# Performance work log

Measured on AMD Instinct MI355X. Metric: run time of the kernel, lower is better.

The kernel has to match this reference:

```python
import math
import jax, jax.numpy as jnp
import numpy as np

B, LA, LB, H = 16, 1024, 1024, 512
NEG = -10000000.0


def setup_inputs() -> dict:
    key = jax.random.key(0)
    k1, k2, k3, k4 = jax.random.split(key, 4)
    a = jax.random.normal(k1, (B, LA, H), dtype=jnp.float32)
    b = jax.random.normal(k2, (B, LB, H), dtype=jnp.float32)
    mask_a = jax.random.randint(k3, (B, LA, 1), 0, 2, dtype=jnp.int32)
    mask_b = jax.random.randint(k4, (B, LB, 1), 0, 2, dtype=jnp.int32)
    temperature = jnp.asarray(1.0 / math.sqrt(H), dtype=jnp.float32)
    return {"a": a, "b": b, "mask_a": mask_a, "mask_b": mask_b, "temperature": temperature}


def reference(a, b, mask_a, mask_b, temperature):
    # attn[b,i,j] = <a_i, b_j> * temperature  -> [B, LA, LB]
    attn = jnp.einsum("bid,bjd->bij", a, b) * temperature
    # pairwise validity mask: outer product of per-token masks
    mask = jnp.einsum("bik,bjk->bij", mask_a.astype(jnp.float32), mask_b.astype(jnp.float32)) > 0
    attn = jnp.where(mask, attn, NEG)
    attn_a = jax.nn.softmax(attn, axis=1)  # softmax over a-tokens
    attn_b = jax.nn.softmax(attn, axis=2)  # softmax over b-tokens
    feature_b = jnp.einsum("bij,bid->bjd", attn_a, a)  # [B, LB, H]
    feature_a = jnp.einsum("bij,bjd->bid", attn_b, b)  # [B, LA, H]
    return (feature_a, feature_b)
```

## Files before the change

### kernel.cpp

```cpp
#include <hip/hip_runtime.h>
#include <hip/hip_bf16.h>

#define NB_ 16
#define LA_ 1024
#define LB_ 1024
#define H_  512

typedef __attribute__((ext_vector_type(8))) short short8;
typedef __attribute__((ext_vector_type(4))) float f32x4;

using bf16 = __hip_bfloat16;

__device__ __forceinline__ float bf2f(unsigned short u) {
    union { unsigned int i; float f; } c; c.i = ((unsigned)u) << 16; return c.f;
}
__device__ __forceinline__ unsigned short f2bf(float f) {
    bf16 h = __float2bfloat16(f);
    return *(unsigned short*)&h;
}

__device__ __forceinline__ void load_lds16(const void* g, void* l) {
    __builtin_amdgcn_global_load_lds(
        (const __attribute__((address_space(1))) void*)g,
        (__attribute__((address_space(3))) void*)l, 16, 0, 0);
}

template<int DB, int MODE>
__device__ __forceinline__ void gemm_tile_cnt(
    const unsigned short* __restrict__ gA, const unsigned short* __restrict__ gB,
    int lda, int ldb, size_t ko,
    unsigned short* lds, char* lA, char* lB,
    const int* aoff, const int* boff, f32x4 acc[4][8])
{
    const char* bA = (const char*)lds + DB * 32768;
    const char* bB = (const char*)lds + 65536 + DB * 32768;
    const int nxt = (DB ^ 1) * 32768;
    short8 av[4][2];
#pragma unroll
    for (int p = 0; p < 4; ++p) {
        if (p == 0) {
#pragma unroll
            for (int f = 0; f < 4; f++)
#pragma unroll
                for (int kk = 0; kk < 2; kk++)
                    av[f][kk] = *(const short8*)(bA + (aoff[f] ^ (kk << 6)));
        }
        short8 bv[2][2];
#pragma unroll
        for (int f = 0; f < 2; f++)
#pragma unroll
            for (int kk = 0; kk < 2; kk++)
                bv[f][kk] = *(const short8*)(bB + (boff[p * 2 + f] ^ (kk << 6)));
        if (MODE == 0) {
            if (p == 0) {
                load_lds16(gA + ko,                       lA + nxt);
                load_lds16(gA + ko + (size_t)64 * lda,    lA + nxt + 8192);
            } else if (p == 1) {
                load_lds16(gA + ko + (size_t)128 * lda,   lA + nxt + 16384);
                load_lds16(gA + ko + (size_t)192 * lda,   lA + nxt + 24576);
            } else if (p == 2) {
                load_lds16(gB + ko,                       lB + nxt);
                load_lds16(gB + ko + (size_t)128 * ldb,   lB + nxt + 16384);
            } else {
                load_lds16(gB + ko + (size_t)64 * ldb,    lB + nxt + 8192);
                load_lds16(gB + ko + (size_t)192 * ldb,   lB + nxt + 24576);
            }
        }
        __builtin_amdgcn_s_barrier();
        __builtin_amdgcn_s_setprio(1);
#pragma unroll
        for (int kk = 0; kk < 2; kk++)
#pragma unroll
            for (int f = 0; f < 2; f++)
#pragma unroll
                for (int m = 0; m < 4; m++)
                    acc[m][p * 2 + f] =
                        __builtin_amdgcn_mfma_f32_16x16x32_bf16(
                            av[m][kk], bv[f][kk], acc[m][p * 2 + f], 0, 0, 0);
        __builtin_amdgcn_s_setprio(0);
        if (p == 1) {
            if (MODE == 0) asm volatile("s_waitcnt vmcnt(4)" ::: "memory");
            else           asm volatile("s_waitcnt vmcnt(0)" ::: "memory");
        }
        if (p == 3 && MODE == 0) asm volatile("s_waitcnt vmcnt(2)" ::: "memory");
        if (p < 3 || MODE == 0) __builtin_amdgcn_s_barrier();
    }
}

__device__ __forceinline__ void gemm_core256(
    const unsigned short* __restrict__ A, const unsigned short* __restrict__ B,
    int lda, int ldb, int K,
    unsigned short* lds, f32x4 acc[4][8])
{
    const int t = threadIdx.x;
    const int w = t >> 6, lane = t & 63;
    const int wr = w >> 1, wc = w & 1;
    const int lm = lane & 15, q = lane >> 4;

    int aoff[4], boff[8];
#pragma unroll
    for (int f = 0; f < 4; f++) {
        const int ra = wr * 64 + f * 16 + lm;
        aoff[f] = ra * 128 + ((q ^ (ra & 7)) << 4);
    }
#pragma unroll
    for (int f = 0; f < 8; f++) {
        const int rb = wc * 128 + f * 16 + lm;
        boff[f] = rb * 128 + ((q ^ (rb & 7)) << 4);
    }

    const int rstep = w * 8 + (lane >> 3);
    const int sc = (lane & 7) ^ (lane >> 3);
    const unsigned short* gA = A + (size_t)rstep * lda + sc * 8;
    const unsigned short* gB = B + (size_t)rstep * ldb + sc * 8;
    char* lA = (char*)lds + w * 1024;
    char* lB = (char*)lds + 65536 + w * 1024;
    const int NT = K >> 6;

    load_lds16(gA,                       lA);
    load_lds16(gA + (size_t)64 * lda,    lA + 8192);
    load_lds16(gA + (size_t)128 * lda,   lA + 16384);
    load_lds16(gA + (size_t)192 * lda,   lA + 24576);
    load_lds16(gB,                       lB);
    load_lds16(gB + (size_t)128 * ldb,   lB + 16384);
    load_lds16(gB + (size_t)64 * ldb,    lB + 8192);
    load_lds16(gB + (size_t)192 * ldb,   lB + 24576);
    asm volatile("s_waitcnt vmcnt(2)" ::: "memory");
    __builtin_amdgcn_s_barrier();
    int kt = 0;
    for (; kt + 2 < NT; kt += 2) {
        gemm_tile_cnt<0, 0>(gA, gB, lda, ldb, (size_t)(kt + 1) * 64,
                            lds, lA, lB, aoff, boff, acc);
        gemm_tile_cnt<1, 0>(gA, gB, lda, ldb, (size_t)(kt + 2) * 64,
                            lds, lA, lB, aoff, boff, acc);
    }
    gemm_tile_cnt<0, 0>(gA, gB, lda, ldb, (size_t)(NT - 1) * 64,
                        lds, lA, lB, aoff, boff, acc);
    gemm_tile_cnt<1, 1>(gA, gB, lda, ldb, 0, lds, lA, lB, aoff, boff, acc);
    __syncthreads();
}

__global__ __launch_bounds__(512, 2) void k_gemm_attn(
    const unsigned short* __restrict__ a_bf, const unsigned short* __restrict__ b_bf,
    const int* __restrict__ mask_a, const int* __restrict__ mask_b,
    const float* __restrict__ temp_p,
    unsigned short* __restrict__ E, unsigned short* __restrict__ ET,
    float* __restrict__ l_row, float* __restrict__ l_col)
{
    __shared__ unsigned short lds[65536];

    const int g = blockIdx.x;
    const int batch = g & 15;
    const int qq = g >> 4;
    const int i0 = (qq >> 2) * 256, j0 = (qq & 3) * 256;

    const unsigned short* A = a_bf + (size_t)batch * LA_ * H_ + (size_t)i0 * H_;
    const unsigned short* B = b_bf + (size_t)batch * LB_ * H_ + (size_t)j0 * H_;
    f32x4 acc[4][8];
#pragma unroll
    for (int x = 0; x < 4; x++)
#pragma unroll
        for (int y = 0; y < 8; y++) acc[x][y] = 0;

    gemm_core256(A, B, H_, H_, H_, lds, acc);

    const float temp = temp_p[0];
    const int t = threadIdx.x, w = t >> 6, lane = t & 63;
    const int wr = w >> 1, wc = w & 1, lm = lane & 15, q = lane >> 4;
    const int* map = mask_a + batch * LA_;
    const int* mbp = mask_b + batch * LB_;
    unsigned short* Ep  = E  + (size_t)batch * LA_ * LB_;
    unsigned short* ETp = ET + (size_t)batch * LB_ * LA_;
    float* lrp = l_row + batch * LA_;
    float* lcp = l_col + batch * LB_;

    int mb8[8];
#pragma unroll
    for (int fn = 0; fn < 8; fn++) mb8[fn] = mbp[j0 + wc * 128 + fn * 16 + lm];

#pragma unroll
    for (int fm = 0; fm < 4; fm++) {
        const int ilb = wr * 64 + fm * 16 + q * 4;
        int ma[4];
#pragma unroll
        for (int r = 0; r < 4; r++) ma[r] = map[i0 + ilb + r];
#pragma unroll
        for (int fn = 0; fn < 8; fn++) {
            const int jl = wc * 128 + fn * 16 + lm;
#pragma unroll
            for (int r = 0; r < 4; r++) {
                const float e = (ma[r] && mb8[fn]) ? __expf(acc[fm][fn][r] * temp) : 0.0f;
                acc[fm][fn][r] = e;
                const int il = ilb + r;
                lds[il * 256 + ((((jl >> 3) ^ ((il >> 1) & 15)) << 3) | (jl & 7))] = f2bf(e);
            }
        }
    }

#pragma unroll
    for (int fm = 0; fm < 4; fm++)
#pragma unroll
        for (int r = 0; r < 4; r++) {
            float s = 0.0f;
#pragma unroll
            for (int fn = 0; fn < 8; fn++) s += acc[fm][fn][r];
            s += __shfl_xor(s, 1, 16); s += __shfl_xor(s, 2, 16);
            s += __shfl_xor(s, 4, 16); s += __shfl_xor(s, 8, 16);
            if (lm == 0) atomicAdd(&lrp[i0 + wr * 64 + fm * 16 + q * 4 + r], s);
        }
#pragma unroll
    for (int fn = 0; fn < 8; fn++) {
        float s = 0.0f;
#pragma unroll
        for (int fm = 0; fm < 4; fm++)
#pragma unroll
            for (int r = 0; r < 4; r++) s += acc[fm][fn][r];
        s += __shfl_xor(s, 16, 64); s += __shfl_xor(s, 32, 64);
        if (lane < 16) atomicAdd(&lcp[j0 + wc * 128 + fn * 16 + lm], s);
    }

    __syncthreads();
#pragma unroll
    for (int rep = 0; rep < 16; rep++) {
        const int il = (t >> 5) + rep * 16;
        const int c = t & 31;
        const int phys = c ^ ((il >> 1) & 15);
        short8 v = *(const short8*)(lds + il * 256 + phys * 8);
        *(short8*)(Ep + (size_t)(i0 + il) * LB_ + j0 + c * 8) = v;
    }

    __syncthreads();
#pragma unroll
    for (int fm = 0; fm < 4; fm++) {
        const int ilb = wr * 64 + fm * 16 + q * 4;
        const int chunk = ilb >> 3, sub = ilb & 7;
#pragma unroll
        for (int fn = 0; fn < 8; fn++) {
            const int jl = wc * 128 + fn * 16 + lm;
            ushort4 pk;
            unsigned short* pp = (unsigned short*)&pk;
#pragma unroll
            for (int r = 0; r < 4; r++) pp[r] = f2bf(acc[fm][fn][r]);
            *(ushort4*)(lds + jl * 256 + (((chunk ^ ((jl >> 1) & 15)) << 3) | sub)) = pk;
        }
    }
    __syncthreads();
#pragma unroll
    for (int rep = 0; rep < 16; rep++) {
        const int jl = (t >> 5) + rep * 16;
        const int c = t & 31;
        const int phys = c ^ ((jl >> 1) & 15);
        short8 v = *(const short8*)(lds + jl * 256 + phys * 8);
        *(short8*)(ETp + (size_t)(j0 + jl) * LA_ + i0 + c * 8) = v;
    }
}

__global__ __launch_bounds__(512, 2) void k_gemm_feat(
    const unsigned short* __restrict__ E, const unsigned short* __restrict__ ET,
    const unsigned short* __restrict__ aT, const unsigned short* __restrict__ bT,
    const int* __restrict__ mask_a, const int* __restrict__ mask_b,
    const int* __restrict__ nA, const int* __restrict__ nB,
    const float* __restrict__ l_row, const float* __restrict__ l_col,
    const float* __restrict__ mean_a, const float* __restrict__ mean_b,
    float* __restrict__ out)
{
    __shared__ unsigned short lds[65536];

    const int g = blockIdx.x;
    const int zc = g & 31;
    const int qq = g >> 5;
    const int n0 = (qq & 1) * 256, m0 = (qq >> 1) * 256;

    const int batch = zc & 15;
    const bool isA = zc < 16;
    const unsigned short* Amat = (isA ? E : ET) + (size_t)batch * 1024 * 1024;
    const unsigned short* Bm   = (isA ? bT : aT) + (size_t)batch * H_ * 1024;
    const int* mp   = (isA ? mask_a : mask_b) + batch * 1024;
    const int nn    = (isA ? nB : nA)[batch];
    const float* sp = (isA ? l_row : l_col) + batch * 1024;
    const float* mv = (isA ? mean_b : mean_a) + batch * H_;
    float* op = out + (isA ? (size_t)0 : (size_t)NB_ * LA_ * H_) + (size_t)batch * 1024 * H_;

    f32x4 acc[4][8];
#pragma unroll
    for (int x = 0; x < 4; x++)
#pragma unroll
        for (int y = 0; y < 8; y++) acc[x][y] = 0;

    gemm_core256(Amat + (size_t)m0 * 1024, Bm + (size_t)n0 * 1024,
                 1024, 1024, 1024, lds, acc);

    const int t = threadIdx.x, w = t >> 6, lane = t & 63;
    const int wr = w >> 1, wc = w & 1, lm = lane & 15, q = lane >> 4;

    float mval[8];
#pragma unroll
    for (int fn = 0; fn < 8; fn++) mval[fn] = mv[n0 + wc * 128 + fn * 16 + lm];

#pragma unroll
    for (int fm = 0; fm < 4; fm++) {
        const int ib = m0 + wr * 64 + fm * 16 + q * 4;
#pragma unroll
        for (int r = 0; r < 4; r++) {
            const int i = ib + r;
            const bool valid = (mp[i] != 0) && (nn > 0);
            const float inv = valid ? 1.0f / sp[i] : 0.0f;
#pragma unroll
            for (int fn = 0; fn < 8; fn++) {
                const int d = n0 + wc * 128 + fn * 16 + lm;
                op[(size_t)i * H_ + d] = valid ? acc[fm][fn][r] * inv : mval[fn];
            }
        }
    }
}

__global__ __launch_bounds__(256) void k_prep(
    const float* __restrict__ a, const float* __restrict__ b,
    unsigned short* __restrict__ aN, unsigned short* __restrict__ bN,
    unsigned short* __restrict__ aT, unsigned short* __restrict__ bT,
    float* __restrict__ mean_a, float* __restrict__ mean_b,
    const int* __restrict__ mask_a, const int* __restrict__ mask_b,
    int* __restrict__ nA, int* __restrict__ nB,
    float* __restrict__ zero_base)
{
    const int g = blockIdx.x, t = threadIdx.x;
    if (g >= 256) {
        const int s = g - 256;
        *(float4*)(zero_base + ((size_t)s * 256 + t) * 4) = make_float4(0, 0, 0, 0);
        const int batch = s & 15, which = s >> 4;
        const int* m = (which ? mask_b : mask_a) + batch * 1024;
        int cnt = m[t] + m[t + 256] + m[t + 512] + m[t + 768];
        __shared__ int red[256];
        red[t] = cnt;
        __syncthreads();
        for (int off = 128; off; off >>= 1) {
            if (t < off) red[t] += red[t + off];
            __syncthreads();
        }
        if (t == 0) (which ? nB : nA)[batch] = red[0];
        return;
    }
    const int dstrip = g & 7, batch = (g >> 3) & 15, sel = g >> 7;
    const float* src = (sel ? b : a) + (size_t)batch * 1024 * H_;
    unsigned short* np = (sel ? bN : aN) + (size_t)batch * 1024 * H_;
    unsigned short* tp = (sel ? bT : aT) + (size_t)batch * H_ * 1024;
    float* mdst = (sel ? mean_b : mean_a) + batch * H_;
    const int d0 = dstrip * 64;

    __shared__ unsigned short lds[64][68];
    __shared__ float cs[4][64];
    const int c4 = (t & 15) * 4;
    float colsum[4] = {0.f, 0.f, 0.f, 0.f};
    for (int i0 = 0; i0 < 1024; i0 += 64) {
#pragma unroll
        for (int it = 0; it < 4; it++) {
            const int r = (t >> 4) + it * 16;
            float4 v = *(const float4*)(src + (size_t)(i0 + r) * H_ + d0 + c4);
            colsum[0] += v.x; colsum[1] += v.y; colsum[2] += v.z; colsum[3] += v.w;
            ushort4 u = make_ushort4(f2bf(v.x), f2bf(v.y), f2bf(v.z), f2bf(v.w));
            *(ushort4*)(np + (size_t)(i0 + r) * H_ + d0 + c4) = u;
            *(ushort4*)&lds[r][c4] = u;
        }
        __syncthreads();
#pragma unroll
        for (int it = 0; it < 4; it++) {
            const int dd = (t >> 4) + it * 16;
            const int i4 = (t & 15) * 4;
            ushort4 u = make_ushort4(lds[i4][dd], lds[i4 + 1][dd],
                                     lds[i4 + 2][dd], lds[i4 + 3][dd]);
            *(ushort4*)(tp + (size_t)(d0 + dd) * 1024 + i0 + i4) = u;
        }
        __syncthreads();
    }
#pragma unroll
    for (int j = 0; j < 4; j++) {
        colsum[j] += __shfl_xor(colsum[j], 16, 64);
        colsum[j] += __shfl_xor(colsum[j], 32, 64);
    }
    const int w = t >> 6, lane = t & 63;
    if (lane < 16) {
#pragma unroll
        for (int j = 0; j < 4; j++) cs[w][c4 + j] = colsum[j];
    }
    __syncthreads();
    if (t < 64) mdst[d0 + t] = (cs[0][t] + cs[1][t] + cs[2][t] + cs[3][t]) * (1.0f / 1024.0f);
}

extern "C" void kernel_launch(void* const* d_in, const int* in_sizes, int n_in,
                              void* d_out, int out_size, void* d_ws, size_t ws_size,
                              hipStream_t stream)
{
    const float* a      = (const float*)d_in[0];
    const float* b      = (const float*)d_in[1];
    const int*   mask_a = (const int*)d_in[2];
    const int*   mask_b = (const int*)d_in[3];
    const float* temp   = (const float*)d_in[4];
    float* out = (float*)d_out;

    char* ws = (char*)d_ws;
    size_t off = 0;
    unsigned short* E    = (unsigned short*)(ws + off); off += (size_t)NB_ * LA_ * LB_ * 2;
    unsigned short* ET   = (unsigned short*)(ws + off); off += (size_t)NB_ * LB_ * LA_ * 2;
    unsigned short* a_bf = (unsigned short*)(ws + off); off += (size_t)NB_ * LA_ * H_ * 2;
    unsigned short* b_bf = (unsigned short*)(ws + off); off += (size_t)NB_ * LB_ * H_ * 2;
    unsigned short* aT   = (unsigned short*)(ws + off); off += (size_t)NB_ * H_ * LA_ * 2;
    unsigned short* bT   = (unsigned short*)(ws + off); off += (size_t)NB_ * H_ * LB_ * 2;
    float* l_row  = (float*)(ws + off); off += (size_t)NB_ * LA_ * 4;
    float* l_col  = (float*)(ws + off); off += (size_t)NB_ * LB_ * 4;
    float* mean_a = (float*)(ws + off); off += (size_t)NB_ * H_ * 4;
    float* mean_b = (float*)(ws + off); off += (size_t)NB_ * H_ * 4;
    int*   nA     = (int*)(ws + off); off += 64;
    int*   nB     = (int*)(ws + off); off += 64;

    k_prep<<<dim3(288), 256, 0, stream>>>(
        a, b, a_bf, b_bf, aT, bT, mean_a, mean_b,
        mask_a, mask_b, nA, nB, l_row);

    k_gemm_attn<<<dim3(256), 512, 0, stream>>>(
        a_bf, b_bf, mask_a, mask_b, temp, E, ET, l_row, l_col);

    k_gemm_feat<<<dim3(256), 512, 0, stream>>>(
        E, ET, aT, bT, mask_a, mask_b, nA, nB, l_row, l_col, mean_a, mean_b, out);
}
```

Measured before the change: 199.7 us.

## Issue all next-tile prefetches at tile start and change transpose LDS swizzle

Moves the global-to-LDS prefetch of the next K tile from being spread across the four MFMA phases to a single burst at the start of each tile, followed by one wait and barrier, and removes the per-phase vmcnt waits. The aim is to make the prefetch schedule simpler and to give memory more lead time. In exchange, the load issue is less interleaved with MFMA work and each tile gains an extra barrier. Separately, the XOR swizzle used in the transposed epilogue store is changed from (jl>>1)&15 to jl&15, to reduce LDS bank conflicts when writing the transposed output.

```diff
diff --git a/kernel.cpp b/kernel.cpp
--- a/kernel.cpp
+++ b/kernel.cpp
@@ -35,6 +35,17 @@
     const char* bA = (const char*)lds + DB * 32768;
     const char* bB = (const char*)lds + 65536 + DB * 32768;
     const int nxt = (DB ^ 1) * 32768;
+    if (MODE == 0) {
+#pragma unroll
+        for (int s = 0; s < 4; s++) {
+            load_lds16(gA + ko + (size_t)(s * 64) * lda, lA + nxt + s * 8192);
+            load_lds16(gB + ko + (size_t)(s * 64) * ldb, lB + nxt + s * 8192);
+        }
+        asm volatile("s_waitcnt vmcnt(8)" ::: "memory");
+    } else {
+        asm volatile("s_waitcnt vmcnt(0)" ::: "memory");
+    }
+    __builtin_amdgcn_s_barrier();
     short8 av[4][2];
 #pragma unroll
     for (int p = 0; p < 4; ++p) {
@@ -51,21 +62,6 @@
 #pragma unroll
             for (int kk = 0; kk < 2; kk++)
                 bv[f][kk] = *(const short8*)(bB + (boff[p * 2 + f] ^ (kk << 6)));
-        if (MODE == 0) {
-            if (p == 0) {
-                load_lds16(gA + ko,                       lA + nxt);
-                load_lds16(gA + ko + (size_t)64 * lda,    lA + nxt + 8192);
-            } else if (p == 1) {
-                load_lds16(gA + ko + (size_t)128 * lda,   lA + nxt + 16384);
-                load_lds16(gA + ko + (size_t)192 * lda,   lA + nxt + 24576);
-            } else if (p == 2) {
-                load_lds16(gB + ko,                       lB + nxt);
-                load_lds16(gB + ko + (size_t)128 * ldb,   lB + nxt + 16384);
-            } else {
-                load_lds16(gB + ko + (size_t)64 * ldb,    lB + nxt + 8192);
-                load_lds16(gB + ko + (size_t)192 * ldb,   lB + nxt + 24576);
-            }
-        }
         __builtin_amdgcn_s_barrier();
         __builtin_amdgcn_s_setprio(1);
 #pragma unroll
@@ -78,12 +74,7 @@
                         __builtin_amdgcn_mfma_f32_16x16x32_bf16(
                             av[m][kk], bv[f][kk], acc[m][p * 2 + f], 0, 0, 0);
         __builtin_amdgcn_s_setprio(0);
-        if (p == 1) {
-            if (MODE == 0) asm volatile("s_waitcnt vmcnt(4)" ::: "memory");
-            else           asm volatile("s_waitcnt vmcnt(0)" ::: "memory");
-        }
-        if (p == 3 && MODE == 0) asm volatile("s_waitcnt vmcnt(2)" ::: "memory");
-        if (p < 3 || MODE == 0) __builtin_amdgcn_s_barrier();
+        __builtin_amdgcn_s_barrier();
     }
 }
 
@@ -117,16 +108,11 @@
     char* lB = (char*)lds + 65536 + w * 1024;
     const int NT = K >> 6;
 
-    load_lds16(gA,                       lA);
-    load_lds16(gA + (size_t)64 * lda,    lA + 8192);
-    load_lds16(gA + (size_t)128 * lda,   lA + 16384);
-    load_lds16(gA + (size_t)192 * lda,   lA + 24576);
-    load_lds16(gB,                       lB);
-    load_lds16(gB + (size_t)128 * ldb,   lB + 16384);
-    load_lds16(gB + (size_t)64 * ldb,    lB + 8192);
-    load_lds16(gB + (size_t)192 * ldb,   lB + 24576);
-    asm volatile("s_waitcnt vmcnt(2)" ::: "memory");
-    __builtin_amdgcn_s_barrier();
+#pragma unroll
+    for (int s = 0; s < 4; s++) {
+        load_lds16(gA + (size_t)(s * 64) * lda, lA + s * 8192);
+        load_lds16(gB + (size_t)(s * 64) * ldb, lB + s * 8192);
+    }
     int kt = 0;
     for (; kt + 2 < NT; kt += 2) {
         gemm_tile_cnt<0, 0>(gA, gB, lda, ldb, (size_t)(kt + 1) * 64,
@@ -241,7 +227,7 @@
             unsigned short* pp = (unsigned short*)&pk;
 #pragma unroll
             for (int r = 0; r < 4; r++) pp[r] = f2bf(acc[fm][fn][r]);
-            *(ushort4*)(lds + jl * 256 + (((chunk ^ ((jl >> 1) & 15)) << 3) | sub)) = pk;
+            *(ushort4*)(lds + jl * 256 + (((chunk ^ (jl & 15)) << 3) | sub)) = pk;
         }
     }
     __syncthreads();
@@ -249,7 +235,7 @@
     for (int rep = 0; rep < 16; rep++) {
         const int jl = (t >> 5) + rep * 16;
         const int c = t & 31;
-        const int phys = c ^ ((jl >> 1) & 15);
+        const int phys = c ^ (jl & 15);
         short8 v = *(const short8*)(lds + jl * 256 + phys * 8);
         *(short8*)(ETp + (size_t)(j0 + jl) * LA_ + i0 + c * 8) = v;
     }
```

Result: slower. 210.3 us (+5.3%).
